# Kernel tuning notes

Hardware: AMD Instinct MI355X
Metric: run time of the kernel (lower is better)

The kernel has to match this reference:

```python
import jax, jax.numpy as jnp
import numpy as np

N_NODES = 100000
N_EDGES = 1600000
N_GRAPHS = 2000
IN_DIM, HID, OUT_DIM, N_CLS = 6, 256, 128, 60
EPS = 1e-5


def setup_inputs() -> dict:
    key = jax.random.key(0)
    ks = jax.random.split(key, 16)
    def lin(k, i, o):
        s = 1.0 / np.sqrt(i)
        k1, k2 = jax.random.split(k)
        return (jax.random.uniform(k1, (i, o), jnp.float32, -s, s),
                jax.random.uniform(k2, (o,), jnp.float32, -s, s))
    W_emb, b_emb = lin(ks[0], IN_DIM, HID)
    Wc1, bc1 = lin(ks[1], HID, HID)
    W2, b2 = lin(ks[2], HID, HID)
    Wc2, bc2 = lin(ks[3], HID, HID)
    W3, b3 = lin(ks[4], HID, OUT_DIM)
    Wcls, bcls = lin(ks[5], OUT_DIM, N_CLS)
    return {
        'node_features': jax.random.normal(ks[6], (N_NODES, IN_DIM), jnp.float32),
        'src': jax.random.randint(ks[7], (N_EDGES,), 0, N_NODES, jnp.int32),
        'dst': jax.random.randint(ks[8], (N_EDGES,), 0, N_NODES, jnp.int32),
        'graph_ids': jnp.sort(jax.random.randint(ks[9], (N_NODES,), 0, N_GRAPHS, jnp.int32)),
        'W_emb': W_emb, 'b_emb': b_emb,
        'Wc1': Wc1, 'bc1': bc1,
        'g1': jnp.ones((HID,), jnp.float32), 'be1': jnp.zeros((HID,), jnp.float32),
        'W2': W2, 'b2': b2,
        'Wc2': Wc2, 'bc2': bc2,
        'g2': jnp.ones((HID,), jnp.float32), 'be2': jnp.zeros((HID,), jnp.float32),
        'W3': W3, 'b3': b3,
        'Wcls': Wcls, 'bcls': bcls,
    }


def _graph_conv(x, W, b, src, dst, dout_isqrt, din_isqrt):
    # DGL GraphConv, norm='both': msg = x_src * dout^-1/2, sum to dst, * din^-1/2, then W, b
    m = x[src] * dout_isqrt[src][:, None]            # [E, H]
    agg = jax.ops.segment_sum(m, dst, num_segments=N_NODES)
    agg = agg * din_isqrt[:, None]
    return agg @ W + b


def _bn(h, g, b):
    # BatchNorm1d, training mode: batch stats over node dim, biased variance
    mu = jnp.mean(h, axis=0)
    var = jnp.mean(jnp.square(h - mu), axis=0)
    return (h - mu) * jax.lax.rsqrt(var + EPS) * g + b


def reference(node_features, src, dst, graph_ids, W_emb, b_emb, Wc1, bc1, g1, be1,
              W2, b2, Wc2, bc2, g2, be2, W3, b3, Wcls, bcls):
    ones_e = jnp.ones((N_EDGES,), jnp.float32)
    dout = jax.ops.segment_sum(ones_e, src, num_segments=N_NODES)
    din = jax.ops.segment_sum(ones_e, dst, num_segments=N_NODES)
    dout_isqrt = jnp.where(dout > 0, jax.lax.rsqrt(jnp.maximum(dout, 1.0)), 0.0)
    din_isqrt = jnp.where(din > 0, jax.lax.rsqrt(jnp.maximum(din, 1.0)), 0.0)

    x = node_features @ W_emb + b_emb                              # [N, H]
    h = x + _graph_conv(x, Wc1, bc1, src, dst, dout_isqrt, din_isqrt)
    h = jax.nn.relu(_bn(h, g1, be1))
    h = h @ W2 + b2
    h = x + _graph_conv(h, Wc2, bc2, src, dst, dout_isqrt, din_isqrt)
    h = jax.nn.relu(_bn(h, g2, be2))
    h = h @ W3 + b3                                                # [N, OUT_DIM]

    # dgl.mean_nodes: per-graph mean of h
    sums = jax.ops.segment_sum(h, graph_ids, num_segments=N_GRAPHS)
    cnts = jax.ops.segment_sum(jnp.ones((N_NODES,), jnp.float32), graph_ids, num_segments=N_GRAPHS)
    y = sums / jnp.maximum(cnts, 1.0)[:, None]                     # [G, OUT_DIM]
    label = y @ Wcls + bcls                                        # [G, N_CLS]
    return h, label
```

## Files before the change

### kernel.cpp

```cpp
#include <hip/hip_runtime.h>

#define NNODES 100000
#define MPAD   100032
#define NEDGES 1600000
#define NGRAPHS 2000
#define HID 256
#define OUTD 128
#define NCLS 60
#define BN_EPS 1e-5f
#define NROWBLK 1563
#define NSCANBLK 98
#define REDBLK 32

typedef __attribute__((ext_vector_type(8))) short bf16x8;
typedef __attribute__((ext_vector_type(4))) float f32x4;

__device__ __forceinline__ float b2f(unsigned short b) {
    unsigned int u = ((unsigned int)b) << 16;
    return __builtin_bit_cast(float, u);
}
__device__ __forceinline__ unsigned short f2b(float f) {
    unsigned int u = __builtin_bit_cast(unsigned int, f);
    u = (u + 0x7FFFu + ((u >> 16) & 1u)) >> 16;
    return (unsigned short)u;
}

__global__ void k_zero_int(int* __restrict__ p, int n) {
    int i = blockIdx.x * blockDim.x + threadIdx.x;
    if (i < n) p[i] = 0;
}

__global__ void k_deg2(const int* __restrict__ src, const int* __restrict__ dst,
                       int* __restrict__ dout, int* __restrict__ din,
                       int* __restrict__ lpos) {
    int e = blockIdx.x * blockDim.x + threadIdx.x;
    if (e < NEDGES) {
        atomicAdd(&dout[src[e]], 1);
        lpos[e] = atomicAdd(&din[dst[e]], 1);
    }
}

__global__ void k_blk_sum(const int* __restrict__ din, const int* __restrict__ dout,
                          int* __restrict__ bsum, float* __restrict__ dos,
                          float* __restrict__ dis) {
    __shared__ int red[256];
    int blk = blockIdx.x, tid = threadIdx.x;
    int base = blk * 1024;
    int s = 0;
#pragma unroll
    for (int j = 0; j < 4; ++j) {
        int i = base + tid + j * 256;
        if (i < NNODES) {
            int b = din[i];
            int a = dout[i];
            s += b;
            dos[i] = a > 0 ? 1.0f / sqrtf((float)a) : 0.0f;
            dis[i] = b > 0 ? 1.0f / sqrtf((float)b) : 0.0f;
        }
    }
    red[tid] = s;
    __syncthreads();
    for (int off = 128; off > 0; off >>= 1) {
        if (tid < off) red[tid] += red[tid + off];
        __syncthreads();
    }
    if (tid == 0) bsum[blk] = red[0];
}

__global__ void k_scan_bsum(int* __restrict__ bsum) {
    if (threadIdx.x == 0) {
        int acc = 0;
        for (int i = 0; i < NSCANBLK; ++i) { int v = bsum[i]; bsum[i] = acc; acc += v; }
    }
}

__global__ void k_scan_local(const int* __restrict__ deg, const int* __restrict__ bsum,
                             int* __restrict__ row_ptr) {
    __shared__ int buf[1024];
    int blk = blockIdx.x, tid = threadIdx.x;
    int i = blk * 1024 + tid;
    int v = (i < NNODES) ? deg[i] : 0;
    buf[tid] = v;
    __syncthreads();
    for (int off = 1; off < 1024; off <<= 1) {
        int t = (tid >= off) ? buf[tid - off] : 0;
        __syncthreads();
        buf[tid] += t;
        __syncthreads();
    }
    int inc = buf[tid] + bsum[blk];
    if (i < NNODES) row_ptr[i + 1] = inc;
    if (i == 0) row_ptr[0] = 0;
}

__global__ void k_place(const int* __restrict__ src, const int* __restrict__ dst,
                        const int* __restrict__ lpos, const int* __restrict__ row_ptr,
                        int* __restrict__ csr_e) {
    int e = blockIdx.x * blockDim.x + threadIdx.x;
    if (e < NEDGES) csr_e[row_ptr[dst[e]] + lpos[e]] = src[e];
}

__global__ void k_nf7(const float* __restrict__ nf, const float* __restrict__ dos,
                      float* __restrict__ nf7) {
    int n = blockIdx.x * blockDim.x + threadIdx.x;
    if (n >= NNODES) return;
    float w = dos[n];
    const float* p = nf + (size_t)n * 6;
    float4 lo = {p[0] * w, p[1] * w, p[2] * w, p[3] * w};
    float4 hi = {p[4] * w, p[5] * w, w, 0.f};
    float4* o = (float4*)(nf7 + (size_t)n * 8);
    o[0] = lo; o[1] = hi;
}

__global__ void k_wconv3(const float* __restrict__ W2, const float* __restrict__ Wc2,
                         const float* __restrict__ W3, unsigned short* __restrict__ Wt2,
                         unsigned short* __restrict__ Wtc2, unsigned short* __restrict__ Wt3) {
    int idx = blockIdx.x * 256 + threadIdx.x;
    if (idx < 65536) {
        int n = idx >> 8, k = idx & 255;
        Wt2[idx] = f2b(W2[k * 256 + n]);
    } else if (idx < 131072) {
        int j = idx - 65536;
        int n = j >> 8, k = j & 255;
        Wtc2[j] = f2b(Wc2[k * 256 + n]);
    } else if (idx < 163840) {
        int j = idx - 131072;
        int n = j >> 8, k = j & 255;
        Wt3[j] = f2b(W3[k * 128 + n]);
    }
}

__global__ void k_small_mm(const float* __restrict__ Wemb, const float* __restrict__ bemb,
                           const float* __restrict__ Wc1, float* __restrict__ M1,
                           float* __restrict__ v1) {
    int c = threadIdx.x;
    int bi = blockIdx.x;
    float acc = 0.f;
    if (bi < 6) {
        for (int k = 0; k < HID; ++k) acc = fmaf(Wemb[bi * HID + k], Wc1[k * HID + c], acc);
        M1[bi * HID + c] = acc;
    } else {
        for (int k = 0; k < HID; ++k) acc = fmaf(bemb[k], Wc1[k * HID + c], acc);
        v1[c] = acc;
    }
}

__global__ void k_agg6(const int* __restrict__ row_ptr, const int* __restrict__ csr_e,
                       const float* __restrict__ nf7, float* __restrict__ t7) {
    int n = blockIdx.x * blockDim.x + threadIdx.x;
    if (n >= NNODES) return;
    float a0 = 0, a1 = 0, a2 = 0, a3 = 0, a4 = 0, a5 = 0, a6 = 0;
    int s = row_ptr[n], e = row_ptr[n + 1];
    int i = s;
    for (; i + 2 <= e; i += 2) {
        const float4* p0 = (const float4*)(nf7 + (size_t)csr_e[i] * 8);
        const float4* p1 = (const float4*)(nf7 + (size_t)csr_e[i + 1] * 8);
        float4 l0 = p0[0], h0 = p0[1], l1 = p1[0], h1 = p1[1];
        a0 += l0.x; a1 += l0.y; a2 += l0.z; a3 += l0.w; a4 += h0.x; a5 += h0.y; a6 += h0.z;
        a0 += l1.x; a1 += l1.y; a2 += l1.z; a3 += l1.w; a4 += h1.x; a5 += h1.y; a6 += h1.z;
    }
    if (i < e) {
        const float4* p0 = (const float4*)(nf7 + (size_t)csr_e[i] * 8);
        float4 l0 = p0[0], h0 = p0[1];
        a0 += l0.x; a1 += l0.y; a2 += l0.z; a3 += l0.w; a4 += h0.x; a5 += h0.y; a6 += h0.z;
    }
    float4* o = (float4*)(t7 + (size_t)n * 8);
    o[0] = make_float4(a0, a1, a2, a3);
    o[1] = make_float4(a4, a5, a6, 0.f);
}

__global__ __launch_bounds__(256) void k_layer1(
    const float* __restrict__ nf, const float* __restrict__ Wemb, const float* __restrict__ bemb,
    const float* __restrict__ M1, const float* __restrict__ v1, const float* __restrict__ bc1,
    const float* __restrict__ t7, const float* __restrict__ dis,
    unsigned short* __restrict__ H, float* __restrict__ psum, float* __restrict__ psq) {
    __shared__ float s_nf[64][6];
    __shared__ float s_t7[64][8];
    __shared__ float s_r[64];
    int blk = blockIdx.x;
    int n0 = blk * 64;
    int tid = threadIdx.x;
    for (int t = tid; t < 384; t += 256) {
        int nl = t / 6, i = t % 6;
        int n = n0 + nl;
        s_nf[nl][i] = (n < NNODES) ? nf[(size_t)n * 6 + i] : 0.f;
    }
    if (tid < 128)
        ((float4*)s_t7)[tid] = ((const float4*)(t7 + (size_t)n0 * 8))[tid];
    if (tid < 64) {
        int n = n0 + tid;
        s_r[tid] = (n < NNODES) ? dis[n] : 0.f;
    }
    int c = tid;
    float wc[6], mc[6];
#pragma unroll
    for (int i = 0; i < 6; ++i) { wc[i] = Wemb[i * HID + c]; mc[i] = M1[i * HID + c]; }
    float v1c = v1[c];
    float bsum = bemb[c] + bc1[c];
    __syncthreads();
    float ps = 0.f, pq = 0.f;
    int nmax = min(64, NNODES - n0);
    for (int nl = 0; nl < nmax; ++nl) {
        float nfd = 0.f, td = 0.f;
#pragma unroll
        for (int i = 0; i < 6; ++i) {
            nfd = fmaf(s_nf[nl][i], wc[i], nfd);
            td = fmaf(s_t7[nl][i], mc[i], td);
        }
        float val = nfd + s_r[nl] * (td + s_t7[nl][6] * v1c) + bsum;
        H[(size_t)(n0 + nl) * HID + c] = f2b(val);
        ps += val;
        pq = fmaf(val, val, pq);
    }
    for (int nl = nmax; nl < 64; ++nl) H[(size_t)(n0 + nl) * HID + c] = 0;
    psum[blk * HID + c] = ps;
    psq[blk * HID + c] = pq;
}

__global__ void k_bn_part(const float* __restrict__ psum, const float* __restrict__ psq,
                          double* __restrict__ tmp) {
    int c = threadIdx.x;
    int s = blockIdx.x;
    double a = 0.0, b = 0.0;
    for (int bb = s; bb < NROWBLK; bb += REDBLK) {
        a += psum[bb * HID + c];
        b += psq[bb * HID + c];
    }
    tmp[s * HID + c] = a;
    tmp[(REDBLK + s) * HID + c] = b;
}

__global__ void k_bn_final(const double* __restrict__ tmp, const float* __restrict__ g,
                           const float* __restrict__ be, float* __restrict__ scale,
                           float* __restrict__ shift) {
    int c = threadIdx.x;
    double s = 0.0, q = 0.0;
    for (int i = 0; i < REDBLK; ++i) { s += tmp[i * HID + c]; q += tmp[(REDBLK + i) * HID + c]; }
    double mu = s / (double)NNODES;
    double var = q / (double)NNODES - mu * mu;
    if (var < 0.0) var = 0.0;
    double inv = 1.0 / sqrt(var + (double)BN_EPS);
    float sc = (float)((double)g[c] * inv);
    scale[c] = sc;
    shift[c] = be[c] - (float)mu * sc;
}

template <int NC, bool ATRANS, bool XEPI, bool PART, bool OUTF32, bool RS>
__global__ __launch_bounds__(256, 2) void k_mgemm(
    const unsigned short* __restrict__ A, const unsigned short* __restrict__ Bt,
    const float* __restrict__ bias,
    const float* __restrict__ scale, const float* __restrict__ shift,
    const float* __restrict__ nf, const float* __restrict__ Wemb, const float* __restrict__ bemb,
    const float* __restrict__ rs,
    unsigned short* __restrict__ Cb, float* __restrict__ Cf,
    float* __restrict__ psum, float* __restrict__ psq) {
    __shared__ unsigned short As[64 * 256];
    __shared__ unsigned short Bs[64 * 256];
    __shared__ float sSc[HID];
    __shared__ float sSh[HID];
    __shared__ float sNf[64][6];
    __shared__ float sXW[6][HID];
    __shared__ float sRs[64];
    __shared__ float redS[2][64];
    __shared__ float redQ[2][64];

    int tid = threadIdx.x;
    int rb = blockIdx.x;
    int row0 = rb * 64;

    if (ATRANS) { sSc[tid] = scale[tid]; sSh[tid] = shift[tid]; }
    if (RS && tid < 64) {
        int n = row0 + tid;
        sRs[tid] = (n < NNODES) ? rs[n] : 0.f;
    }
    if (XEPI) {
        for (int t = tid; t < 6 * NC; t += 256) {
            int i = t / NC, cl = t % NC;
            sXW[i][cl] = Wemb[i * HID + cl];
        }
        if (tid < 64) {
            int n = row0 + tid;
#pragma unroll
            for (int i = 0; i < 6; ++i) sNf[tid][i] = (n < NNODES) ? nf[(size_t)n * 6 + i] : 0.f;
        }
    }
    if (ATRANS) __syncthreads();

#pragma unroll
    for (int i = 0; i < 8; ++i) {
        int g = i * 256 + tid;
        int row = g >> 5, kc = g & 31;
        uint4 v = *(const uint4*)(A + (size_t)(row0 + row) * 256 + kc * 8);
        if (ATRANS) {
            unsigned int w[4] = {v.x, v.y, v.z, v.w};
#pragma unroll
            for (int q = 0; q < 4; ++q) {
                int k0 = kc * 8 + q * 2;
                float f0 = b2f((unsigned short)(w[q] & 0xffffu));
                float f1 = b2f((unsigned short)(w[q] >> 16));
                f0 = fmaxf(fmaf(f0, sSc[k0], sSh[k0]), 0.f);
                f1 = fmaxf(fmaf(f1, sSc[k0 + 1], sSh[k0 + 1]), 0.f);
                w[q] = (unsigned int)f2b(f0) | ((unsigned int)f2b(f1) << 16);
            }
            v.x = w[0]; v.y = w[1]; v.z = w[2]; v.w = w[3];
        }
        int pkc = kc ^ (row & 7);
        *(uint4*)(&As[row * 256 + pkc * 8]) = v;
    }

    int w = tid >> 6, lane = tid & 63;
    int wm = w >> 1, wn = w & 1;
    int lrow = lane & 15, lk = lane >> 4;

    for (int cb = 0; cb < NC / 64; ++cb) {
        int c0 = cb * 64;
        if (cb) __syncthreads();
#pragma unroll
        for (int i = 0; i < 8; ++i) {
            int g = i * 256 + tid;
            int row = g >> 5, kc = g & 31;
            uint4 v = *(const uint4*)(Bt + (size_t)(c0 + row) * 256 + kc * 8);
            int pkc = kc ^ (row & 7);
            *(uint4*)(&Bs[row * 256 + pkc * 8]) = v;
        }
        __syncthreads();

        f32x4 acc[2][2] = {};
#pragma unroll
        for (int ks = 0; ks < 8; ++ks) {
            bf16x8 af[2], bfr[2];
#pragma unroll
            for (int fm = 0; fm < 2; ++fm) {
                int r = wm * 32 + fm * 16 + lrow;
                int kc = ks * 4 + lk;
                af[fm] = *(const bf16x8*)(&As[r * 256 + (kc ^ (r & 7)) * 8]);
            }
#pragma unroll
            for (int fn = 0; fn < 2; ++fn) {
                int r = wn * 32 + fn * 16 + lrow;
                int kc = ks * 4 + lk;
                bfr[fn] = *(const bf16x8*)(&Bs[r * 256 + (kc ^ (r & 7)) * 8]);
            }
#pragma unroll
            for (int fm = 0; fm < 2; ++fm)
#pragma unroll
                for (int fn = 0; fn < 2; ++fn)
                    acc[fm][fn] = __builtin_amdgcn_mfma_f32_16x16x32_bf16(af[fm], bfr[fn], acc[fm][fn], 0, 0, 0);
        }

        float pS[2] = {0.f, 0.f}, pQ[2] = {0.f, 0.f};
#pragma unroll
        for (int fn = 0; fn < 2; ++fn) {
            int cl = wn * 32 + fn * 16 + lrow;
            int gc = c0 + cl;
            float bv = bias[gc];
            if (XEPI) bv += bemb[gc];
#pragma unroll
            for (int fm = 0; fm < 2; ++fm) {
#pragma unroll
                for (int r = 0; r < 4; ++r) {
                    int rl = wm * 32 + fm * 16 + lk * 4 + r;
                    int gr = row0 + rl;
                    float val = acc[fm][fn][r] + bv;
                    if (XEPI) {
#pragma unroll
                        for (int l = 0; l < 6; ++l) val = fmaf(sNf[rl][l], sXW[l][gc], val);
                    }
                    if (RS) val *= sRs[rl];
                    if (gr < NNODES) {
                        if (OUTF32) Cf[(size_t)gr * NC + gc] = val;
                        else        Cb[(size_t)gr * NC + gc] = f2b(val);
                        if (PART) { pS[fn] += val; pQ[fn] = fmaf(val, val, pQ[fn]); }
                    }
                }
            }
        }
        if (PART) {
#pragma unroll
            for (int fn = 0; fn < 2; ++fn) {
                float s = pS[fn], q = pQ[fn];
                s += __shfl_xor(s, 16); s += __shfl_xor(s, 32);
                q += __shfl_xor(q, 16); q += __shfl_xor(q, 32);
                if (lk == 0) {
                    int cl = wn * 32 + fn * 16 + lrow;
                    redS[wm][cl] = s;
                    redQ[wm][cl] = q;
                }
            }
            __syncthreads();
            if (tid < 64) {
                psum[(size_t)rb * HID + c0 + tid] = redS[0][tid] + redS[1][tid];
                psq [(size_t)rb * HID + c0 + tid] = redQ[0][tid] + redQ[1][tid];
            }
        }
    }
}

#define ADD8(vv) { \
    a[0] += b2f((unsigned short)(vv.x & 0xffffu)); \
    a[1] += b2f((unsigned short)(vv.x >> 16)); \
    a[2] += b2f((unsigned short)(vv.y & 0xffffu)); \
    a[3] += b2f((unsigned short)(vv.y >> 16)); \
    a[4] += b2f((unsigned short)(vv.z & 0xffffu)); \
    a[5] += b2f((unsigned short)(vv.z >> 16)); \
    a[6] += b2f((unsigned short)(vv.w & 0xffffu)); \
    a[7] += b2f((unsigned short)(vv.w >> 16)); }

__global__ __launch_bounds__(256) void k_agg(const int* __restrict__ row_ptr,
                                             const int* __restrict__ csr_e,
                                             const unsigned short* __restrict__ X,
                                             const float* __restrict__ dis,
                                             unsigned short* __restrict__ out) {
    int wid = threadIdx.x >> 6, lane = threadIdx.x & 63;
    int half = lane >> 5, l32 = lane & 31;
    int n = blockIdx.x * 4 + wid;
    if (n >= NNODES) return;
    int s = row_ptr[n], e = row_ptr[n + 1];
    float a[8] = {0.f, 0.f, 0.f, 0.f, 0.f, 0.f, 0.f, 0.f};
    int i = s;
    for (; i + 8 <= e; i += 8) {
        int s0 = csr_e[i + half];
        int s1 = csr_e[i + 2 + half];
        int s2 = csr_e[i + 4 + half];
        int s3 = csr_e[i + 6 + half];
        uint4 v0 = ((const uint4*)(X + (size_t)s0 * HID))[l32];
        uint4 v1 = ((const uint4*)(X + (size_t)s1 * HID))[l32];
        uint4 v2 = ((const uint4*)(X + (size_t)s2 * HID))[l32];
        uint4 v3 = ((const uint4*)(X + (size_t)s3 * HID))[l32];
        ADD8(v0) ADD8(v1) ADD8(v2) ADD8(v3)
    }
    for (; i + 2 <= e; i += 2) {
        int s0 = csr_e[i + half];
        uint4 v0 = ((const uint4*)(X + (size_t)s0 * HID))[l32];
        ADD8(v0)
    }
    if (i < e && half == 0) {
        int s0 = csr_e[i];
        uint4 v0 = ((const uint4*)(X + (size_t)s0 * HID))[l32];
        ADD8(v0)
    }
#pragma unroll
    for (int j = 0; j < 8; ++j) a[j] += __shfl_xor(a[j], 32);
    if (half == 0) {
        float r = dis[n];
        uint4 o;
        o.x = (unsigned)f2b(a[0] * r) | ((unsigned)f2b(a[1] * r) << 16);
        o.y = (unsigned)f2b(a[2] * r) | ((unsigned)f2b(a[3] * r) << 16);
        o.z = (unsigned)f2b(a[4] * r) | ((unsigned)f2b(a[5] * r) << 16);
        o.w = (unsigned)f2b(a[6] * r) | ((unsigned)f2b(a[7] * r) << 16);
        ((uint4*)(out + (size_t)n * HID))[l32] = o;
    }
}

__global__ __launch_bounds__(128) void k_mean_label(const float* __restrict__ Hout,
                                                    const int* __restrict__ gids,
                                                    const float* __restrict__ Wcls,
                                                    const float* __restrict__ bcls,
                                                    float* __restrict__ lab) {
    int g = blockIdx.x;
    int c = threadIdx.x;
    int lo = 0, hi = NNODES;
    while (lo < hi) { int mid = (lo + hi) >> 1; if (gids[mid] < g) lo = mid + 1; else hi = mid; }
    int s = lo;
    hi = NNODES;
    while (lo < hi) { int mid = (lo + hi) >> 1; if (gids[mid] < g + 1) lo = mid + 1; else hi = mid; }
    int e = lo;
    float acc = 0.f;
    for (int n = s; n < e; ++n) acc += Hout[(size_t)n * OUTD + c];
    int cnt = e - s;
    float y = acc / (float)max(cnt, 1);
    __shared__ float ys[OUTD];
    ys[c] = y;
    __syncthreads();
    if (c < NCLS) {
        float a = bcls[c];
        for (int k = 0; k < OUTD; ++k) a = fmaf(ys[k], Wcls[k * NCLS + c], a);
        lab[(size_t)g * NCLS + c] = a;
    }
}

extern "C" void kernel_launch(void* const* d_in, const int* in_sizes, int n_in,
                              void* d_out, int out_size, void* d_ws, size_t ws_size,
                              hipStream_t stream) {
    const float* nf   = (const float*)d_in[0];
    const int*   src  = (const int*)d_in[1];
    const int*   dst  = (const int*)d_in[2];
    const int*   gids = (const int*)d_in[3];
    const float* Wemb = (const float*)d_in[4];
    const float* bemb = (const float*)d_in[5];
    const float* Wc1  = (const float*)d_in[6];
    const float* bc1  = (const float*)d_in[7];
    const float* g1   = (const float*)d_in[8];
    const float* be1  = (const float*)d_in[9];
    const float* W2   = (const float*)d_in[10];
    const float* b2   = (const float*)d_in[11];
    const float* Wc2  = (const float*)d_in[12];
    const float* bc2  = (const float*)d_in[13];
    const float* g2   = (const float*)d_in[14];
    const float* be2  = (const float*)d_in[15];
    const float* W3   = (const float*)d_in[16];
    const float* b3   = (const float*)d_in[17];
    const float* Wcls = (const float*)d_in[18];
    const float* bcls = (const float*)d_in[19];

    float* out_h   = (float*)d_out;
    float* out_lab = out_h + (size_t)NNODES * OUTD;

    float* ws = (float*)d_ws;
    size_t off = 0;
    auto take = [&](size_t n) { float* p = ws + off; off += (n + 63) & ~(size_t)63; return p; };
    unsigned short* actA = (unsigned short*)take((size_t)MPAD * HID / 2);
    unsigned short* actB = (unsigned short*)take((size_t)MPAD * HID / 2);
    unsigned short* Wt2  = (unsigned short*)take(HID * HID / 2);
    unsigned short* Wtc2 = (unsigned short*)take(HID * HID / 2);
    unsigned short* Wt3  = (unsigned short*)take(OUTD * HID / 2);
    int*   deg_out = (int*)take(NNODES);
    int*   deg_in  = (int*)take(NNODES);
    float* dout_is = take(NNODES);
    float* din_is  = take(NNODES);
    int*   row_ptr = (int*)take(NNODES + 1);
    int*   lpos    = (int*)take(NEDGES);
    int*   csr_e   = (int*)take(NEDGES);
    float* nf7     = take((size_t)NNODES * 8);
    float* t7      = take((size_t)MPAD * 8);
    float* M1      = take(6 * HID);
    float* v1      = take(HID);
    float* psum    = take((size_t)NROWBLK * HID);
    float* psq     = take((size_t)NROWBLK * HID);
    float* scale1  = take(HID);
    float* shift1  = take(HID);
    float* scale2  = take(HID);
    float* shift2  = take(HID);
    int*   bsum    = (int*)take(128);
    double* bn_tmp = (double*)take(2 * 2 * REDBLK * HID);

    k_zero_int<<<(2 * 100032 + 255) / 256, 256, 0, stream>>>(deg_out, 2 * 100032);
    k_deg2<<<(NEDGES + 255) / 256, 256, 0, stream>>>(src, dst, deg_out, deg_in, lpos);
    k_blk_sum<<<NSCANBLK, 256, 0, stream>>>(deg_in, deg_out, bsum, dout_is, din_is);
    k_scan_bsum<<<1, 64, 0, stream>>>(bsum);
    k_scan_local<<<NSCANBLK, 1024, 0, stream>>>(deg_in, bsum, row_ptr);
    k_place<<<(NEDGES + 255) / 256, 256, 0, stream>>>(src, dst, lpos, row_ptr, csr_e);
    k_nf7<<<(NNODES + 255) / 256, 256, 0, stream>>>(nf, dout_is, nf7);
    k_wconv3<<<640, 256, 0, stream>>>(W2, Wc2, W3, Wt2, Wtc2, Wt3);
    k_small_mm<<<7, 256, 0, stream>>>(Wemb, bemb, Wc1, M1, v1);
    k_agg6<<<(NNODES + 255) / 256, 256, 0, stream>>>(row_ptr, csr_e, nf7, t7);
    k_layer1<<<NROWBLK, 256, 0, stream>>>(nf, Wemb, bemb, M1, v1, bc1, t7, din_is,
                                          actA, psum, psq);
    k_bn_part<<<REDBLK, 256, 0, stream>>>(psum, psq, bn_tmp);
    k_bn_final<<<1, 256, 0, stream>>>(bn_tmp, g1, be1, scale1, shift1);
    k_mgemm<HID, true, false, false, false, true><<<NROWBLK, 256, 0, stream>>>(
        actA, Wt2, b2, scale1, shift1, nullptr, nullptr, nullptr, dout_is,
        actB, nullptr, nullptr, nullptr);
    k_agg<<<NNODES / 4, 256, 0, stream>>>(row_ptr, csr_e, actB, din_is, actA);
    k_mgemm<HID, false, true, true, false, false><<<NROWBLK, 256, 0, stream>>>(
        actA, Wtc2, bc2, nullptr, nullptr, nf, Wemb, bemb, nullptr,
        actB, nullptr, psum, psq);
    k_bn_part<<<REDBLK, 256, 0, stream>>>(psum, psq, bn_tmp);
    k_bn_final<<<1, 256, 0, stream>>>(bn_tmp, g2, be2, scale2, shift2);
    k_mgemm<OUTD, true, false, false, true, false><<<NROWBLK, 256, 0, stream>>>(
        actB, Wt3, b3, scale2, shift2, nullptr, nullptr, nullptr, nullptr,
        nullptr, out_h, nullptr, nullptr);
    k_mean_label<<<NGRAPHS, OUTD, 0, stream>>>(out_h, gids, Wcls, bcls, out_lab);
}
```

Measured before the change: 720.8 us.

## Pad degree counters, fuse prep kernels, and alias workspace buffers

```diff
diff --git a/kernel.cpp b/kernel.cpp
--- a/kernel.cpp
+++ b/kernel.cpp
@@ -11,6 +11,7 @@
 #define NROWBLK 1563
 #define NSCANBLK 98
 #define REDBLK 32
+#define DPAD 16
 
 typedef __attribute__((ext_vector_type(8))) short bf16x8;
 typedef __attribute__((ext_vector_type(4))) float f32x4;
@@ -25,18 +26,22 @@
     return (unsigned short)u;
 }
 
-__global__ void k_zero_int(int* __restrict__ p, int n) {
+__global__ void k_zero4(int4* __restrict__ p, int n4) {
     int i = blockIdx.x * blockDim.x + threadIdx.x;
-    if (i < n) p[i] = 0;
-}
-
-__global__ void k_deg2(const int* __restrict__ src, const int* __restrict__ dst,
-                       int* __restrict__ dout, int* __restrict__ din,
-                       int* __restrict__ lpos) {
-    int e = blockIdx.x * blockDim.x + threadIdx.x;
-    if (e < NEDGES) {
-        atomicAdd(&dout[src[e]], 1);
-        lpos[e] = atomicAdd(&din[dst[e]], 1);
+    if (i < n4) p[i] = make_int4(0, 0, 0, 0);
+}
+
+__global__ __launch_bounds__(256) void k_deg2(
+        const int* __restrict__ src, const int* __restrict__ dst,
+        int* __restrict__ dout, int* __restrict__ din, int* __restrict__ lpos) {
+    int t = blockIdx.x * 256 + threadIdx.x;
+#pragma unroll
+    for (int j = 0; j < 4; ++j) {
+        int e = t + j * 400128;
+        if (e < NEDGES) {
+            atomicAdd(&dout[src[e] * DPAD], 1);
+            lpos[e] = atomicAdd(&din[dst[e] * DPAD], 1);
+        }
     }
 }
 
@@ -51,8 +56,8 @@
     for (int j = 0; j < 4; ++j) {
         int i = base + tid + j * 256;
         if (i < NNODES) {
-            int b = din[i];
-            int a = dout[i];
+            int b = din[i * DPAD];
+            int a = dout[i * DPAD];
             s += b;
             dos[i] = a > 0 ? 1.0f / sqrtf((float)a) : 0.0f;
             dis[i] = b > 0 ? 1.0f / sqrtf((float)b) : 0.0f;
@@ -79,7 +84,7 @@
     __shared__ int buf[1024];
     int blk = blockIdx.x, tid = threadIdx.x;
     int i = blk * 1024 + tid;
-    int v = (i < NNODES) ? deg[i] : 0;
+    int v = (i < NNODES) ? deg[i * DPAD] : 0;
     buf[tid] = v;
     __syncthreads();
     for (int off = 1; off < 1024; off <<= 1) {
@@ -100,48 +105,50 @@
     if (e < NEDGES) csr_e[row_ptr[dst[e]] + lpos[e]] = src[e];
 }
 
-__global__ void k_nf7(const float* __restrict__ nf, const float* __restrict__ dos,
-                      float* __restrict__ nf7) {
-    int n = blockIdx.x * blockDim.x + threadIdx.x;
-    if (n >= NNODES) return;
-    float w = dos[n];
-    const float* p = nf + (size_t)n * 6;
-    float4 lo = {p[0] * w, p[1] * w, p[2] * w, p[3] * w};
-    float4 hi = {p[4] * w, p[5] * w, w, 0.f};
-    float4* o = (float4*)(nf7 + (size_t)n * 8);
-    o[0] = lo; o[1] = hi;
-}
-
-__global__ void k_wconv3(const float* __restrict__ W2, const float* __restrict__ Wc2,
-                         const float* __restrict__ W3, unsigned short* __restrict__ Wt2,
-                         unsigned short* __restrict__ Wtc2, unsigned short* __restrict__ Wt3) {
-    int idx = blockIdx.x * 256 + threadIdx.x;
-    if (idx < 65536) {
-        int n = idx >> 8, k = idx & 255;
-        Wt2[idx] = f2b(W2[k * 256 + n]);
-    } else if (idx < 131072) {
-        int j = idx - 65536;
-        int n = j >> 8, k = j & 255;
-        Wtc2[j] = f2b(Wc2[k * 256 + n]);
-    } else if (idx < 163840) {
-        int j = idx - 131072;
-        int n = j >> 8, k = j & 255;
-        Wt3[j] = f2b(W3[k * 128 + n]);
-    }
-}
-
-__global__ void k_small_mm(const float* __restrict__ Wemb, const float* __restrict__ bemb,
-                           const float* __restrict__ Wc1, float* __restrict__ M1,
-                           float* __restrict__ v1) {
-    int c = threadIdx.x;
-    int bi = blockIdx.x;
-    float acc = 0.f;
-    if (bi < 6) {
-        for (int k = 0; k < HID; ++k) acc = fmaf(Wemb[bi * HID + k], Wc1[k * HID + c], acc);
-        M1[bi * HID + c] = acc;
+__global__ void k_prep(const float* __restrict__ nf, const float* __restrict__ dos,
+                       float* __restrict__ nf7,
+                       const float* __restrict__ W2, const float* __restrict__ Wc2,
+                       const float* __restrict__ W3, unsigned short* __restrict__ Wt2,
+                       unsigned short* __restrict__ Wtc2, unsigned short* __restrict__ Wt3,
+                       const float* __restrict__ Wemb, const float* __restrict__ bemb,
+                       const float* __restrict__ Wc1, float* __restrict__ M1,
+                       float* __restrict__ v1) {
+    int blk = blockIdx.x, tid = threadIdx.x;
+    if (blk < 391) {
+        int n = blk * 256 + tid;
+        if (n < NNODES) {
+            float w = dos[n];
+            const float* p = nf + (size_t)n * 6;
+            float4 lo = {p[0] * w, p[1] * w, p[2] * w, p[3] * w};
+            float4 hi = {p[4] * w, p[5] * w, w, 0.f};
+            float4* o = (float4*)(nf7 + (size_t)n * 8);
+            o[0] = lo; o[1] = hi;
+        }
+    } else if (blk < 1031) {
+        int idx = (blk - 391) * 256 + tid;
+        if (idx < 65536) {
+            int n = idx >> 8, k = idx & 255;
+            Wt2[idx] = f2b(W2[k * 256 + n]);
+        } else if (idx < 131072) {
+            int j = idx - 65536;
+            int n = j >> 8, k = j & 255;
+            Wtc2[j] = f2b(Wc2[k * 256 + n]);
+        } else {
+            int j = idx - 131072;
+            int n = j >> 8, k = j & 255;
+            Wt3[j] = f2b(W3[k * 128 + n]);
+        }
     } else {
-        for (int k = 0; k < HID; ++k) acc = fmaf(bemb[k], Wc1[k * HID + c], acc);
-        v1[c] = acc;
+        int bi = blk - 1031;
+        int c = tid;
+        float acc = 0.f;
+        if (bi < 6) {
+            for (int k = 0; k < HID; ++k) acc = fmaf(Wemb[bi * HID + k], Wc1[k * HID + c], acc);
+            M1[bi * HID + c] = acc;
+        } else {
+            for (int k = 0; k < HID; ++k) acc = fmaf(bemb[k], Wc1[k * HID + c], acc);
+            v1[c] = acc;
+        }
     }
 }
 
@@ -185,8 +192,13 @@
         int n = n0 + nl;
         s_nf[nl][i] = (n < NNODES) ? nf[(size_t)n * 6 + i] : 0.f;
     }
-    if (tid < 128)
-        ((float4*)s_t7)[tid] = ((const float4*)(t7 + (size_t)n0 * 8))[tid];
+    if (tid < 128) {
+        int n = n0 + tid / 2;
+        if (n < NNODES)
+            ((float4*)s_t7)[tid] = ((const float4*)(t7 + (size_t)n0 * 8))[tid];
+        else
+            ((float4*)s_t7)[tid] = make_float4(0.f, 0.f, 0.f, 0.f);
+    }
     if (tid < 64) {
         int n = n0 + tid;
         s_r[tid] = (n < NNODES) ? dis[n] : 0.f;
@@ -514,19 +526,14 @@
     unsigned short* Wt2  = (unsigned short*)take(HID * HID / 2);
     unsigned short* Wtc2 = (unsigned short*)take(HID * HID / 2);
     unsigned short* Wt3  = (unsigned short*)take(OUTD * HID / 2);
-    int*   deg_out = (int*)take(NNODES);
-    int*   deg_in  = (int*)take(NNODES);
     float* dout_is = take(NNODES);
     float* din_is  = take(NNODES);
     int*   row_ptr = (int*)take(NNODES + 1);
-    int*   lpos    = (int*)take(NEDGES);
+    float* lpos_t7 = take(NEDGES);
     int*   csr_e   = (int*)take(NEDGES);
-    float* nf7     = take((size_t)NNODES * 8);
-    float* t7      = take((size_t)MPAD * 8);
+    float* nf7_ps  = take(800320);
     float* M1      = take(6 * HID);
     float* v1      = take(HID);
-    float* psum    = take((size_t)NROWBLK * HID);
-    float* psq     = take((size_t)NROWBLK * HID);
     float* scale1  = take(HID);
     float* shift1  = take(HID);
     float* scale2  = take(HID);
@@ -534,15 +541,23 @@
     int*   bsum    = (int*)take(128);
     double* bn_tmp = (double*)take(2 * 2 * REDBLK * HID);
 
-    k_zero_int<<<(2 * 100032 + 255) / 256, 256, 0, stream>>>(deg_out, 2 * 100032);
-    k_deg2<<<(NEDGES + 255) / 256, 256, 0, stream>>>(src, dst, deg_out, deg_in, lpos);
+    int*   deg_out = (int*)actA;
+    int*   deg_in  = deg_out + 100032 * DPAD;
+    int*   lpos    = (int*)lpos_t7;
+    float* t7      = lpos_t7;
+    float* nf7     = nf7_ps;
+    float* psum    = nf7_ps;
+    float* psq     = nf7_ps + 400128;
+
+    k_zero4<<<(2 * 100032 * DPAD / 4 + 255) / 256, 256, 0, stream>>>(
+        (int4*)deg_out, 2 * 100032 * DPAD / 4);
+    k_deg2<<<1563, 256, 0, stream>>>(src, dst, deg_out, deg_in, lpos);
     k_blk_sum<<<NSCANBLK, 256, 0, stream>>>(deg_in, deg_out, bsum, dout_is, din_is);
     k_scan_bsum<<<1, 64, 0, stream>>>(bsum);
     k_scan_local<<<NSCANBLK, 1024, 0, stream>>>(deg_in, bsum, row_ptr);
     k_place<<<(NEDGES + 255) / 256, 256, 0, stream>>>(src, dst, lpos, row_ptr, csr_e);
-    k_nf7<<<(NNODES + 255) / 256, 256, 0, stream>>>(nf, dout_is, nf7);
-    k_wconv3<<<640, 256, 0, stream>>>(W2, Wc2, W3, Wt2, Wtc2, Wt3);
-    k_small_mm<<<7, 256, 0, stream>>>(Wemb, bemb, Wc1, M1, v1);
+    k_prep<<<1038, 256, 0, stream>>>(nf, dout_is, nf7, W2, Wc2, W3, Wt2, Wtc2, Wt3,
+                                     Wemb, bemb, Wc1, M1, v1);
     k_agg6<<<(NNODES + 255) / 256, 256, 0, stream>>>(row_ptr, csr_e, nf7, t7);
     k_layer1<<<NROWBLK, 256, 0, stream>>>(nf, Wemb, bemb, M1, v1, bc1, t7, din_is,
                                           actA, psum, psq);
```

Result: no change. 723.1 us (+0.3%).
